# Kernel optimization log

Measured on AMD Instinct MI355X. Metric: run time of the kernel, lower is better.

## Reference

```python
import jax, jax.numpy as jnp
import numpy as np
import math

B, Hdim, Wdim = 8, 32, 32
CH = [64, 128, 256, 512]
KV = 960


def setup_inputs() -> dict:
    key = jax.random.key(0)
    ks = jax.random.split(key, 24)
    f32 = jnp.float32
    inp = {}
    inp["emb1"] = jax.random.normal(ks[0], (B, CH[0], Hdim, Wdim), f32)
    inp["emb2"] = jax.random.normal(ks[1], (B, CH[1], Hdim, Wdim), f32)
    inp["emb3"] = jax.random.normal(ks[2], (B, CH[2], Hdim, Wdim), f32)
    inp["emb4"] = jax.random.normal(ks[3], (B, CH[3], Hdim, Wdim), f32)
    inp["emb_all"] = jax.random.normal(ks[4], (B, KV, Hdim, Wdim), f32)
    s = 0.05  # small init so softmax/instnorm stay well-conditioned
    inp["w_mhead1"] = jax.random.normal(ks[5], (CH[0], CH[0]), f32) * s
    inp["w_mhead2"] = jax.random.normal(ks[6], (CH[1], CH[1]), f32) * s
    inp["w_mhead3"] = jax.random.normal(ks[7], (CH[2], CH[2]), f32) * s
    inp["w_mhead4"] = jax.random.normal(ks[8], (CH[3], CH[3]), f32) * s
    inp["w_mheadq"] = jax.random.normal(ks[9], (KV, KV), f32) * s
    inp["w_mheadk"] = jax.random.normal(ks[10], (KV, KV), f32) * s
    inp["w_mheadv"] = jax.random.normal(ks[11], (KV, KV), f32) * s
    inp["w_q1"] = jax.random.normal(ks[12], (CH[0], 2, 3, 3), f32) * s
    inp["w_q2"] = jax.random.normal(ks[13], (CH[1], 2, 3, 3), f32) * s
    inp["w_q3"] = jax.random.normal(ks[14], (CH[2], 2, 3, 3), f32) * s
    inp["w_q4"] = jax.random.normal(ks[15], (CH[3], 2, 3, 3), f32) * s
    inp["w_qc"] = jax.random.normal(ks[16], (KV, 1, 3, 3), f32) * s
    inp["w_kc"] = jax.random.normal(ks[17], (KV, 1, 3, 3), f32) * s
    inp["w_vc"] = jax.random.normal(ks[18], (KV, 1, 3, 3), f32) * s
    inp["w_proj1"] = jax.random.normal(ks[19], (CH[0], CH[0]), f32) * s
    inp["w_proj2"] = jax.random.normal(ks[20], (CH[1], CH[1]), f32) * s
    inp["w_proj3"] = jax.random.normal(ks[21], (CH[2], CH[2]), f32) * s
    inp["w_proj4"] = jax.random.normal(ks[22], (CH[3], CH[3]), f32) * s
    return inp


def conv1x1(x, w):
    # x: [b,c,h,w], w: [o,c] (1x1 conv, no bias)
    return jnp.einsum('bchw,oc->bohw', x, w)


def dwconv3x3(x, w, groups):
    # torch grouped conv: w [O, C//g, 3, 3]
    return jax.lax.conv_general_dilated(
        x, w, window_strides=(1, 1), padding='SAME',
        dimension_numbers=('NCHW', 'OIHW', 'NCHW'),
        feature_group_count=groups)


def l2norm(x):
    # F.normalize(dim=-1): divide by max(||x||_2, 1e-12)
    n = jnp.sqrt(jnp.sum(x * x, axis=-1, keepdims=True))
    return x / jnp.maximum(n, 1e-12)


def instnorm(x, eps=1e-5):
    # InstanceNorm2d(head=1, affine=False) on [b, head, c, n]: normalize per (b, head)
    m = jnp.mean(x, axis=(2, 3), keepdims=True)
    v = jnp.var(x, axis=(2, 3), keepdims=True)
    return (x - m) * jax.lax.rsqrt(v + eps)


def reference(emb1, emb2, emb3, emb4, emb_all,
              w_mhead1, w_mhead2, w_mhead3, w_mhead4,
              w_mheadq, w_mheadk, w_mheadv,
              w_q1, w_q2, w_q3, w_q4,
              w_qc, w_kc, w_vc,
              w_proj1, w_proj2, w_proj3, w_proj4):
    b, _, h, w = emb1.shape
    hw = h * w
    scale = 1.0 / math.sqrt(KV)

    # channel cross-attention over the concatenated features
    Qc = dwconv3x3(conv1x1(emb_all, w_mheadq), w_qc, KV).reshape(b, 1, KV, hw)
    Kc = dwconv3x3(conv1x1(emb_all, w_mheadk), w_kc, KV).reshape(b, 1, KV, hw)
    Vc = dwconv3x3(conv1x1(emb_all, w_mheadv), w_vc, KV).reshape(b, 1, KV, hw)
    Qc = l2norm(Qc)
    Kc = l2norm(Kc)
    sim = jnp.einsum('bhcn,bhdn->bhcd', Qc, Kc) * scale  # [b,1,KV,KV]
    sim = jax.nn.softmax(instnorm(sim), axis=-1)
    ctx = jnp.einsum('bhcd,bhdn->bhcn', sim, Vc)  # [b,1,KV,hw]

    def branch(emb, w_mh, w_q, groups, w_proj):
        c = emb.shape[1]
        q = dwconv3x3(conv1x1(emb, w_mh), w_q, groups).reshape(b, 1, c, hw)
        q = l2norm(q)
        attn = jnp.einsum('bhcn,bhdn->bhcd', q, ctx) * scale  # [b,1,c,KV]
        p = jax.nn.softmax(instnorm(attn), axis=-1)
        o = jnp.einsum('bhcd,bhdn->bhcn', p, ctx)  # [b,1,c,hw]
        o = jnp.mean(o, axis=1).reshape(b, c, h, w)
        return conv1x1(o, w_proj)

    O1 = branch(emb1, w_mhead1, w_q1, CH[0] // 2, w_proj1)
    O2 = branch(emb2, w_mhead2, w_q2, CH[1] // 2, w_proj2)
    O3 = branch(emb3, w_mhead3, w_q3, CH[2] // 2, w_proj3)
    O4 = branch(emb4, w_mhead4, w_q4, CH[3] // 2, w_proj4)
    return (O1, O2, O3, O4)
```

## Files before the change

### kernel.cpp

```cpp
#include <hip/hip_runtime.h>
#include <hip/hip_bf16.h>
#include <math.h>

#define NB 8
#define HWN 1024
#define KVC 960

typedef short bf16x8 __attribute__((ext_vector_type(8)));
typedef unsigned short u16x8 __attribute__((ext_vector_type(8)));
typedef float f32x4 __attribute__((ext_vector_type(4)));
typedef unsigned short ushort_t;

__device__ inline ushort_t f2bf(float f) {
    __hip_bfloat16 h = __float2bfloat16(f);
    return *reinterpret_cast<ushort_t*>(&h);
}
__device__ inline float bf2f(ushort_t u) {
    union { float f; unsigned int i; } x; x.i = ((unsigned int)u) << 16; return x.f;
}
__device__ inline int XB(int n) { return ((n & 7) ^ ((n >> 3) & 7)) << 1; }

__device__ inline void glds16(const ushort_t* src, ushort_t* dst) {
    __builtin_amdgcn_global_load_lds(
        (const __attribute__((address_space(1))) void*)src,
        (__attribute__((address_space(3))) void*)dst, 16, 0, 0);
}

struct F2BTab {
    const float* src[16];
    long dstOff[16];
    int nblk[16];
    int nseg;
};

__global__ __launch_bounds__(256)
void f2b_batched(F2BTab tab, ushort_t* base)
{
    int b = blockIdx.x, s = 0;
    while (s < tab.nseg - 1 && b >= tab.nblk[s]) { b -= tab.nblk[s]; ++s; }
    float4 v = *((const float4*)tab.src[s] + (long)b * 256 + threadIdx.x);
    ushort4 o = make_ushort4(f2bf(v.x), f2bf(v.y), f2bf(v.z), f2bf(v.w));
    *((ushort4*)(base + tab.dstOff[s]) + (long)b * 256 + threadIdx.x) = o;
}

__global__ __launch_bounds__(256)
void mfma_gemm_nt_stats(const ushort_t* __restrict__ A, const ushort_t* __restrict__ B,
                        float* __restrict__ C, float2* __restrict__ part,
                        int M, int N, int K, long sA, long sB, long sC, float alpha)
{
    __shared__ __align__(16) ushort_t lA[128 * 64];
    __shared__ __align__(16) ushort_t lB[128 * 64];
    const ushort_t* Ab = A + (long)blockIdx.z * sA;
    const ushort_t* Bb = B + (long)blockIdx.z * sB;
    const int row0 = blockIdx.y * 128, col0 = blockIdx.x * 128;
    const int t = threadIdx.x, lane = t & 63, w = t >> 6;
    const int wr = w >> 1, wc = w & 1;
    const int arl = lane >> 3;
    const int acs = ((lane & 7) ^ arl) * 8;
    int arow[4], brow[4];
    #pragma unroll
    for (int j = 0; j < 4; ++j) {
        int r = row0 + w * 32 + j * 8 + arl;  arow[j] = r < M ? r : M - 1;
        int rb = col0 + w * 32 + j * 8 + arl; brow[j] = rb < N ? rb : N - 1;
    }

    f32x4 acc[4][4];
    #pragma unroll
    for (int m = 0; m < 4; ++m)
        #pragma unroll
        for (int n = 0; n < 4; ++n)
            acc[m][n] = (f32x4){0.f, 0.f, 0.f, 0.f};

    for (int k0 = 0; k0 < K; k0 += 64) {
        #pragma unroll
        for (int j = 0; j < 4; ++j) {
            glds16(Ab + (long)arow[j] * K + k0 + acs, lA + (w * 32 + j * 8) * 64);
            glds16(Bb + (long)brow[j] * K + k0 + acs, lB + (w * 32 + j * 8) * 64);
        }
        __syncthreads();
        #pragma unroll
        for (int sub = 0; sub < 2; ++sub) {
            const int kc = (lane >> 4) + sub * 4;
            bf16x8 aF[4], bF[4];
            #pragma unroll
            for (int m = 0; m < 4; ++m) {
                int rl = wr * 64 + m * 16 + (lane & 15);
                aF[m] = *(const bf16x8*)(lA + rl * 64 + (kc ^ (rl & 7)) * 8);
            }
            #pragma unroll
            for (int n = 0; n < 4; ++n) {
                int rl = wc * 64 + n * 16 + (lane & 15);
                bF[n] = *(const bf16x8*)(lB + rl * 64 + (kc ^ (rl & 7)) * 8);
            }
            #pragma unroll
            for (int m = 0; m < 4; ++m)
                #pragma unroll
                for (int n = 0; n < 4; ++n)
                    acc[m][n] = __builtin_amdgcn_mfma_f32_16x16x32_bf16(aF[m], bF[n], acc[m][n], 0, 0, 0);
        }
        __syncthreads();
    }

    const int cr0 = row0 + wr * 64 + (lane >> 4) * 4;
    const int cc0 = col0 + wc * 64 + (lane & 15);
    float* Cb = C + (long)blockIdx.z * sC;
    float s1 = 0.f, s2 = 0.f;
    #pragma unroll
    for (int m = 0; m < 4; ++m) {
        #pragma unroll
        for (int n = 0; n < 4; ++n) {
            int ccol = cc0 + n * 16;
            if (ccol >= N) continue;
            #pragma unroll
            for (int r = 0; r < 4; ++r) {
                int crow = cr0 + m * 16 + r;
                if (crow < M) {
                    float v = acc[m][n][r] * alpha;
                    Cb[(long)crow * N + ccol] = v;
                    s1 += v; s2 += v * v;
                }
            }
        }
    }
    #pragma unroll
    for (int off = 32; off > 0; off >>= 1) {
        s1 += __shfl_down(s1, off);
        s2 += __shfl_down(s2, off);
    }
    float* rbuf = (float*)lA;
    if (lane == 0) { rbuf[w] = s1; rbuf[4 + w] = s2; }
    __syncthreads();
    if (t == 0)
        part[(blockIdx.z * 8 + blockIdx.y) * 8 + blockIdx.x] =
            make_float2(rbuf[0] + rbuf[1] + rbuf[2] + rbuf[3],
                        rbuf[4] + rbuf[5] + rbuf[6] + rbuf[7]);
}

struct NNTab {
    const ushort_t* A[5];
    const ushort_t* B[5];
    void* C[5];
    long sA[5], sB[5], sC[5];
    int M[5], K[5], obf[5], mt0[5];
    int nseg;
};

__global__ __launch_bounds__(256)
void mfma_gemm_nn(NNTab tab)
{
    __shared__ __align__(16) ushort_t lA[128 * 64];
    __shared__ __align__(16) ushort_t lB[128 * 64];
    int si = 0;
    #pragma unroll
    for (int s = 1; s < 5; ++s)
        if (s < tab.nseg && (int)blockIdx.y >= tab.mt0[s]) si = s;
    const int M = tab.M[si], K = tab.K[si];
    const int ytile = blockIdx.y - tab.mt0[si];
    const ushort_t* Ab = tab.A[si] + (long)blockIdx.z * tab.sA[si];
    const ushort_t* Bb = tab.B[si] + (long)blockIdx.z * tab.sB[si];
    const int row0 = ytile * 128, col0 = blockIdx.x * 128;
    const int t = threadIdx.x, lane = t & 63, w = t >> 6;
    const int wr = w >> 1, wc = w & 1;
    const int arl = lane >> 3;
    const int acs = ((lane & 7) ^ arl) * 8;
    int arow[4];
    #pragma unroll
    for (int j = 0; j < 4; ++j) {
        int r = row0 + w * 32 + j * 8 + arl;
        arow[j] = r < M ? r : M - 1;
    }
    const int n_i = t & 31, k_i = t >> 5;

    f32x4 acc[4][4];
    #pragma unroll
    for (int m = 0; m < 4; ++m)
        #pragma unroll
        for (int n = 0; n < 4; ++n)
            acc[m][n] = (f32x4){0.f, 0.f, 0.f, 0.f};

    for (int k0 = 0; k0 < K; k0 += 64) {
        #pragma unroll
        for (int j = 0; j < 4; ++j)
            glds16(Ab + (long)arow[j] * K + k0 + acs, lA + (w * 32 + j * 8) * 64);
        ushort4 q[8];
        const int gk = k0 + k_i * 8;
        #pragma unroll
        for (int kk = 0; kk < 8; ++kk)
            q[kk] = *(const ushort4*)(Bb + (long)(gk + kk) * 1024 + col0 + n_i * 4);
        #pragma unroll
        for (int i = 0; i < 4; ++i) {
            int n = n_i * 4 + i;
            int cw = (k_i * 2) ^ XB(n);
            u16x8 v;
            #pragma unroll
            for (int kk = 0; kk < 4; ++kk) {
                v[kk]     = ((const ushort_t*)&q[kk])[i];
                v[4 + kk] = ((const ushort_t*)&q[4 + kk])[i];
            }
            *(u16x8*)(lB + n * 64 + cw * 4) = v;
        }
        __syncthreads();
        #pragma unroll
        for (int sub = 0; sub < 2; ++sub) {
            const int kcA = (lane >> 4) + sub * 4;
            const int cB = (lane >> 4) * 2 + sub * 8;
            bf16x8 aF[4], bF[4];
            #pragma unroll
            for (int m = 0; m < 4; ++m) {
                int rl = wr * 64 + m * 16 + (lane & 15);
                aF[m] = *(const bf16x8*)(lA + rl * 64 + (kcA ^ (rl & 7)) * 8);
            }
            #pragma unroll
            for (int n = 0; n < 4; ++n) {
                int nl = wc * 64 + n * 16 + (lane & 15);
                bF[n] = *(const bf16x8*)(lB + nl * 64 + (cB ^ XB(nl)) * 4);
            }
            #pragma unroll
            for (int m = 0; m < 4; ++m)
                #pragma unroll
                for (int n = 0; n < 4; ++n)
                    acc[m][n] = __builtin_amdgcn_mfma_f32_16x16x32_bf16(aF[m], bF[n], acc[m][n], 0, 0, 0);
        }
        __syncthreads();
    }

    const int cr0 = row0 + wr * 64 + (lane >> 4) * 4;
    const int cc0 = col0 + wc * 64 + (lane & 15);
    const int obf = tab.obf[si];
    ushort_t* Cb_b = (ushort_t*)tab.C[si] + (long)blockIdx.z * tab.sC[si];
    float* Cb_f = (float*)tab.C[si] + (long)blockIdx.z * tab.sC[si];
    #pragma unroll
    for (int m = 0; m < 4; ++m) {
        #pragma unroll
        for (int n = 0; n < 4; ++n) {
            int ccol = cc0 + n * 16;
            #pragma unroll
            for (int r = 0; r < 4; ++r) {
                int crow = cr0 + m * 16 + r;
                if (crow < M) {
                    float v = acc[m][n][r];
                    if (obf) Cb_b[(long)crow * 1024 + ccol] = f2bf(v);
                    else     Cb_f[(long)crow * 1024 + ccol] = v;
                }
            }
        }
    }
}

__global__ __launch_bounds__(256)
void stencil_all(const ushort_t* __restrict__ Xqkv, const ushort_t* __restrict__ mh_x,
                 const float* __restrict__ w_qc, const float* __restrict__ w_kc,
                 const float* __restrict__ w_vc,
                 const float* __restrict__ wq1, const float* __restrict__ wq2,
                 const float* __restrict__ wq3, const float* __restrict__ wq4,
                 ushort_t* __restrict__ Qc, ushort_t* __restrict__ Kc,
                 ushort_t* __restrict__ Vc, ushort_t* __restrict__ q_all)
{
    __shared__ float p0[32 * 33];
    __shared__ float p1[32 * 33];
    __shared__ float red[5];
    const int bid = blockIdx.x;
    const int t = threadIdx.x;
    const int i0 = t * 4, y = i0 >> 5, x0 = i0 & 31;

    if (bid < 23040) {
        const int which = bid / 7680;
        const int p = bid - which * 7680;
        const int b = p / 960, c = p - b * 960;
        const ushort_t* ip = Xqkv + ((long)b * 2880 + which * 960 + c) * 1024;
        const float* wgt = (which == 0 ? w_qc : which == 1 ? w_kc : w_vc) + c * 9;
        ushort_t* op = (which == 0 ? Qc : which == 1 ? Kc : Vc) + (long)p * 1024;
        ushort4 u = *(const ushort4*)(ip + i0);
        float* rw = p0 + y * 33 + x0;
        rw[0] = bf2f(u.x); rw[1] = bf2f(u.y); rw[2] = bf2f(u.z); rw[3] = bf2f(u.w);
        __syncthreads();
        float W[9];
        #pragma unroll
        for (int q = 0; q < 9; ++q) W[q] = wgt[q];
        float r[3][6];
        #pragma unroll
        for (int dy = 0; dy < 3; ++dy) {
            int yy = y + dy - 1;
            bool vy = (unsigned)yy < 32u;
            #pragma unroll
            for (int j = 0; j < 6; ++j) {
                int xx = x0 - 1 + j;
                r[dy][j] = (vy && (unsigned)xx < 32u) ? p0[yy * 33 + xx] : 0.f;
            }
        }
        float o[4];
        #pragma unroll
        for (int q = 0; q < 4; ++q)
            o[q] = r[0][q] * W[0] + r[0][q + 1] * W[1] + r[0][q + 2] * W[2]
                 + r[1][q] * W[3] + r[1][q + 1] * W[4] + r[1][q + 2] * W[5]
                 + r[2][q] * W[6] + r[2][q + 1] * W[7] + r[2][q + 2] * W[8];
        float inv = 1.f;
        if (which < 2) {
            float s = o[0] * o[0] + o[1] * o[1] + o[2] * o[2] + o[3] * o[3];
            #pragma unroll
            for (int off = 32; off > 0; off >>= 1) s += __shfl_down(s, off);
            if ((t & 63) == 0) red[t >> 6] = s;
            __syncthreads();
            if (t == 0) red[4] = 1.0f / fmaxf(sqrtf(red[0] + red[1] + red[2] + red[3]), 1e-12f);
            __syncthreads();
            inv = red[4];
        }
        *(ushort4*)(op + i0) =
            make_ushort4(f2bf(o[0] * inv), f2bf(o[1] * inv), f2bf(o[2] * inv), f2bf(o[3] * inv));
        return;
    }
    const int po = bid - 23040;
    const int o = po & 1023, b = po >> 10;
    ushort_t* op = q_all + (long)po * 1024;
    int off; const float* wbase;
    if (o < 64)       { off = 0;   wbase = wq1; }
    else if (o < 128) { *(ushort4*)(op + i0) = make_ushort4(0, 0, 0, 0); return; }
    else if (o < 256) { off = 128; wbase = wq2; }
    else if (o < 512) { off = 256; wbase = wq3; }
    else              { off = 512; wbase = wq4; }
    const int ol = o - off;
    const int g2 = ol & ~1;
    const ushort_t* ip0 = mh_x + ((long)(b << 10) + off + g2) * 1024;
    const ushort_t* ip1 = ip0 + 1024;
    ushort4 u0 = *(const ushort4*)(ip0 + i0);
    ushort4 u1 = *(const ushort4*)(ip1 + i0);
    float* r0w = p0 + y * 33 + x0;
    float* r1w = p1 + y * 33 + x0;
    r0w[0] = bf2f(u0.x); r0w[1] = bf2f(u0.y); r0w[2] = bf2f(u0.z); r0w[3] = bf2f(u0.w);
    r1w[0] = bf2f(u1.x); r1w[1] = bf2f(u1.y); r1w[2] = bf2f(u1.z); r1w[3] = bf2f(u1.w);
    __syncthreads();
    const float* wp = wbase + ol * 18;
    float W[18];
    #pragma unroll
    for (int q = 0; q < 18; ++q) W[q] = wp[q];
    float o4[4] = {0.f, 0.f, 0.f, 0.f};
    #pragma unroll
    for (int pl = 0; pl < 2; ++pl) {
        const float* src = pl ? p1 : p0;
        const float* Wp = W + pl * 9;
        float r[3][6];
        #pragma unroll
        for (int dy = 0; dy < 3; ++dy) {
            int yy = y + dy - 1;
            bool vy = (unsigned)yy < 32u;
            #pragma unroll
            for (int j = 0; j < 6; ++j) {
                int xx = x0 - 1 + j;
                r[dy][j] = (vy && (unsigned)xx < 32u) ? src[yy * 33 + xx] : 0.f;
            }
        }
        #pragma unroll
        for (int q = 0; q < 4; ++q)
            o4[q] += r[0][q] * Wp[0] + r[0][q + 1] * Wp[1] + r[0][q + 2] * Wp[2]
                   + r[1][q] * Wp[3] + r[1][q + 1] * Wp[4] + r[1][q + 2] * Wp[5]
                   + r[2][q] * Wp[6] + r[2][q + 1] * Wp[7] + r[2][q + 2] * Wp[8];
    }
    float s = o4[0] * o4[0] + o4[1] * o4[1] + o4[2] * o4[2] + o4[3] * o4[3];
    #pragma unroll
    for (int off2 = 32; off2 > 0; off2 >>= 1) s += __shfl_down(s, off2);
    if ((t & 63) == 0) red[t >> 6] = s;
    __syncthreads();
    if (t == 0) red[4] = 1.0f / fmaxf(sqrtf(red[0] + red[1] + red[2] + red[3]), 1e-12f);
    __syncthreads();
    float inv = red[4];
    *(ushort4*)(op + i0) =
        make_ushort4(f2bf(o4[0] * inv), f2bf(o4[1] * inv), f2bf(o4[2] * inv), f2bf(o4[3] * inv));
}

__global__ void reduce_sim(const float2* __restrict__ part, float2* __restrict__ stats)
{
    float2 p = part[blockIdx.x * 64 + threadIdx.x];
    float s1 = p.x, s2 = p.y;
    #pragma unroll
    for (int off = 32; off > 0; off >>= 1) {
        s1 += __shfl_down(s1, off);
        s2 += __shfl_down(s2, off);
    }
    if (threadIdx.x == 0) stats[blockIdx.x] = make_float2(s1, s2);
}

__global__ void reduce_branch(const float2* __restrict__ part, float2* __restrict__ stats)
{
    const int br = blockIdx.x & 3, b = blockIdx.x >> 2;
    const int lo4[4] = {0, 1, 2, 4}, hi4[4] = {1, 2, 4, 8};
    float s1 = 0.f, s2 = 0.f;
    if (threadIdx.x < 8) {
        for (int my = lo4[br]; my < hi4[br]; ++my) {
            float2 p = part[(b * 8 + my) * 8 + threadIdx.x];
            s1 += p.x; s2 += p.y;
        }
    }
    #pragma unroll
    for (int off = 32; off > 0; off >>= 1) {
        s1 += __shfl_down(s1, off);
        s2 += __shfl_down(s2, off);
    }
    if (threadIdx.x == 0) stats[b * 4 + br] = make_float2(s1, s2);
}

__global__ __launch_bounds__(256)
void instnorm_softmax_bf16(const float* __restrict__ x, ushort_t* __restrict__ out,
                           const float2* __restrict__ stats, int rowsPerB, float invL)
{
    int row = blockIdx.x;
    int b = row / rowsPerB;
    float2 st = stats[b];
    float mean = st.x * invL;
    float var = st.y * invL - mean * mean;
    float rinv = rsqrtf(var + 1e-5f);
    const float* xr = x + (long)row * 960;
    ushort_t* orow = out + (long)row * 960;
    int t = threadIdx.x;
    float v[4];
    float mx = -1e30f;
    #pragma unroll
    for (int q = 0; q < 4; ++q) {
        int i = t + q * 256;
        if (i < 960) { v[q] = (xr[i] - mean) * rinv; mx = fmaxf(mx, v[q]); }
        else v[q] = -1e30f;
    }
    #pragma unroll
    for (int off = 32; off > 0; off >>= 1) mx = fmaxf(mx, __shfl_down(mx, off));
    __shared__ float rm[4];
    __shared__ float bmax, bsuminv;
    if ((t & 63) == 0) rm[t >> 6] = mx;
    __syncthreads();
    if (t == 0) bmax = fmaxf(fmaxf(rm[0], rm[1]), fmaxf(rm[2], rm[3]));
    __syncthreads();
    float mall = bmax;
    float s = 0.f;
    #pragma unroll
    for (int q = 0; q < 4; ++q) {
        int i = t + q * 256;
        if (i < 960) { v[q] = __expf(v[q] - mall); s += v[q]; }
    }
    #pragma unroll
    for (int off = 32; off > 0; off >>= 1) s += __shfl_down(s, off);
    if ((t & 63) == 0) rm[t >> 6] = s;
    __syncthreads();
    if (t == 0) bsuminv = 1.0f / (rm[0] + rm[1] + rm[2] + rm[3]);
    __syncthreads();
    float invS = bsuminv;
    #pragma unroll
    for (int q = 0; q < 4; ++q) {
        int i = t + q * 256;
        if (i < 960) orow[i] = f2bf(v[q] * invS);
    }
}

__global__ __launch_bounds__(256)
void softmax_attn_kernel(const float* __restrict__ x, ushort_t* __restrict__ P,
                         const float2* __restrict__ stats)
{
    const int r = blockIdx.x & 1023, b = blockIdx.x >> 10;
    const int t = threadIdx.x;
    ushort_t* orow = P + ((long)(b << 10) + r) * 960;
    int br; float cnt;
    if (r < 64)       { br = 0; cnt = 64.f; }
    else if (r < 128) {
        #pragma unroll
        for (int q = 0; q < 4; ++q) {
            int i = t + q * 256;
            if (i < 960) orow[i] = 0;
        }
        return;
    }
    else if (r < 256) { br = 1; cnt = 128.f; }
    else if (r < 512) { br = 2; cnt = 256.f; }
    else              { br = 3; cnt = 512.f; }
    float invL = 1.0f / (cnt * 960.f);
    float2 st = stats[b * 4 + br];
    float mean = st.x * invL;
    float var = st.y * invL - mean * mean;
    float rinv = rsqrtf(var + 1e-5f);
    const float* xr = x + ((long)(b << 10) + r) * 960;
    float v[4];
    float mx = -1e30f;
    #pragma unroll
    for (int q = 0; q < 4; ++q) {
        int i = t + q * 256;
        if (i < 960) { v[q] = (xr[i] - mean) * rinv; mx = fmaxf(mx, v[q]); }
        else v[q] = -1e30f;
    }
    #pragma unroll
    for (int off = 32; off > 0; off >>= 1) mx = fmaxf(mx, __shfl_down(mx, off));
    __shared__ float rm[4];
    __shared__ float bmax, bsuminv;
    if ((t & 63) == 0) rm[t >> 6] = mx;
    __syncthreads();
    if (t == 0) bmax = fmaxf(fmaxf(rm[0], rm[1]), fmaxf(rm[2], rm[3]));
    __syncthreads();
    float mall = bmax;
    float s = 0.f;
    #pragma unroll
    for (int q = 0; q < 4; ++q) {
        int i = t + q * 256;
        if (i < 960) { v[q] = __expf(v[q] - mall); s += v[q]; }
    }
    #pragma unroll
    for (int off = 32; off > 0; off >>= 1) s += __shfl_down(s, off);
    if ((t & 63) == 0) rm[t >> 6] = s;
    __syncthreads();
    if (t == 0) bsuminv = 1.0f / (rm[0] + rm[1] + rm[2] + rm[3]);
    __syncthreads();
    float invS = bsuminv;
    #pragma unroll
    for (int q = 0; q < 4; ++q) {
        int i = t + q * 256;
        if (i < 960) orow[i] = f2bf(v[q] * invS);
    }
}


extern "C" void kernel_launch(void* const* d_in, const int* in_sizes, int n_in,
                              void* d_out, int out_size, void* d_ws, size_t ws_size,
                              hipStream_t stream)
{
    const float* emb[4]  = {(const float*)d_in[0], (const float*)d_in[1],
                            (const float*)d_in[2], (const float*)d_in[3]};
    const float* emb_all = (const float*)d_in[4];
    const float* w_mh[4] = {(const float*)d_in[5], (const float*)d_in[6],
                            (const float*)d_in[7], (const float*)d_in[8]};
    const float* w_mq = (const float*)d_in[9];
    const float* w_mk = (const float*)d_in[10];
    const float* w_mv = (const float*)d_in[11];
    const float* w_q[4] = {(const float*)d_in[12], (const float*)d_in[13],
                           (const float*)d_in[14], (const float*)d_in[15]};
    const float* w_qc = (const float*)d_in[16];
    const float* w_kc = (const float*)d_in[17];
    const float* w_vc = (const float*)d_in[18];
    const float* w_proj[4] = {(const float*)d_in[19], (const float*)d_in[20],
                              (const float*)d_in[21], (const float*)d_in[22]};
    float* out = (float*)d_out;

    char* Wb = (char*)d_ws;
    ushort_t* U = (ushort_t*)d_ws;
    const long eWQKV = 0;
    const long eWMH  = 2764800;
    const long eWPJ  = 3112960;
    const long eEmbA = 3461120;
    const long eEmbI = 11325440;
    const long eXq   = 19189760;
    const long eMhx  = 42782720;
    const long eQc   = 51171328;
    const long eKc   = 59035648;
    const long eVc   = 66899968;
    const long eF6   = eXq;
    const long ePc   = eXq + 15728640;
    const long eQall = eEmbA;
    const long eCtx  = eMhx;
    const long ePall = eQc;
    const long eOall = eKc;
    float2* part  = (float2*)(Wb + 149528576);
    float2* stats = (float2*)(Wb + 149533000);

    ushort_t* WQKVb = U + eWQKV;
    ushort_t* WMHb  = U + eWMH;
    ushort_t* WPJb  = U + eWPJ;
    ushort_t* embB_all = U + eEmbA;
    ushort_t* Xqkv  = U + eXq;
    ushort_t* mh_x  = U + eMhx;
    ushort_t* QcB   = U + eQc;
    ushort_t* KcB   = U + eKc;
    ushort_t* VcB   = U + eVc;
    float*    F6    = (float*)(U + eF6);
    ushort_t* Pc    = U + ePc;
    ushort_t* q_all = U + eQall;
    ushort_t* ctx   = U + eCtx;
    ushort_t* P_all = U + ePall;
    ushort_t* o_all = U + eOall;
    ushort_t* embB_i[4] = {U + eEmbI, U + eEmbI + 524288, U + eEmbI + 1572864, U + eEmbI + 3670016};

    const float scale = 0.0322748612183951400f;
    const long SB = (long)KVC * HWN;
    const long S1024 = 1024L * 1024;
    const int CH[4] = {64, 128, 256, 512};
    const int mhoff[4] = {0, 4096, 20480, 86016};
    const int rowOff[4] = {0, 128, 256, 512};
    const long outOff[4] = {0, 524288, 1572864, 3670016};
    dim3 blk(256);

    F2BTab tf;
    const float* fs[16] = {w_mq, w_mk, w_mv,
                           w_mh[0], w_mh[1], w_mh[2], w_mh[3],
                           w_proj[0], w_proj[1], w_proj[2], w_proj[3],
                           emb_all, emb[0], emb[1], emb[2], emb[3]};
    long fd[16] = {eWQKV, eWQKV + 921600, eWQKV + 1843200,
                   eWMH + 0, eWMH + 4096, eWMH + 20480, eWMH + 86016,
                   eWPJ + 0, eWPJ + 4096, eWPJ + 20480, eWPJ + 86016,
                   eEmbA, eEmbI, eEmbI + 524288, eEmbI + 1572864, eEmbI + 3670016};
    int fn[16] = {900, 900, 900, 4, 16, 64, 256, 4, 16, 64, 256,
                  7680, 512, 1024, 2048, 4096};
    int ftot = 0;
    for (int i = 0; i < 16; ++i) { tf.src[i] = fs[i]; tf.dstOff[i] = fd[i]; tf.nblk[i] = fn[i]; ftot += fn[i]; }
    tf.nseg = 16;
    f2b_batched<<<ftot, blk, 0, stream>>>(tf, U);

    auto nn1 = [&](const ushort_t* A, long sA, const ushort_t* B, long sB,
                   void* C, long sC, int M, int K, int obf) {
        NNTab tb;
        tb.A[0] = A; tb.B[0] = B; tb.C[0] = C;
        tb.sA[0] = sA; tb.sB[0] = sB; tb.sC[0] = sC;
        tb.M[0] = M; tb.K[0] = K; tb.obf[0] = obf; tb.mt0[0] = 0;
        for (int s = 1; s < 5; ++s) { tb.A[s] = A; tb.B[s] = B; tb.C[s] = C; tb.sA[s] = 0; tb.sB[s] = 0; tb.sC[s] = 0; tb.M[s] = M; tb.K[s] = K; tb.obf[s] = obf; tb.mt0[s] = 1 << 30; }
        tb.nseg = 1;
        dim3 g(8, (M + 127) / 128, NB);
        mfma_gemm_nn<<<g, blk, 0, stream>>>(tb);
    };

    {
        NNTab tb;
        tb.A[0] = WQKVb; tb.B[0] = embB_all; tb.C[0] = Xqkv;
        tb.sA[0] = 0; tb.sB[0] = SB; tb.sC[0] = 2880L * 1024;
        tb.M[0] = 2880; tb.K[0] = 960; tb.obf[0] = 1; tb.mt0[0] = 0;
        int mt = 23;
        for (int i = 0; i < 4; ++i) {
            tb.A[1 + i] = WMHb + mhoff[i]; tb.B[1 + i] = embB_i[i];
            tb.C[1 + i] = mh_x + (long)rowOff[i] * 1024;
            tb.sA[1 + i] = 0; tb.sB[1 + i] = (long)CH[i] * 1024; tb.sC[1 + i] = S1024;
            tb.M[1 + i] = CH[i]; tb.K[1 + i] = CH[i]; tb.obf[1 + i] = 1; tb.mt0[1 + i] = mt;
            mt += (CH[i] + 127) / 128;
        }
        tb.nseg = 5;
        dim3 g(8, mt, NB);
        mfma_gemm_nn<<<g, blk, 0, stream>>>(tb);
    }

    stencil_all<<<31232, blk, 0, stream>>>(Xqkv, mh_x, w_qc, w_kc, w_vc,
                                           w_q[0], w_q[1], w_q[2], w_q[3],
                                           QcB, KcB, VcB, q_all);

    mfma_gemm_nt_stats<<<dim3(8, 8, NB), blk, 0, stream>>>(
        QcB, KcB, F6, part, KVC, KVC, HWN, SB, SB, (long)KVC * KVC, scale);
    reduce_sim<<<NB, 64, 0, stream>>>(part, stats);
    instnorm_softmax_bf16<<<NB * KVC, blk, 0, stream>>>(F6, Pc, stats, KVC,
                                                        1.f / ((float)KVC * (float)KVC));

    nn1(Pc, (long)KVC * KVC, VcB, SB, ctx, SB, KVC, KVC, 1);

    mfma_gemm_nt_stats<<<dim3(8, 8, NB), blk, 0, stream>>>(
        q_all, ctx, F6, part, 1024, KVC, HWN, S1024, SB, SB, scale);
    reduce_branch<<<32, 64, 0, stream>>>(part, stats);
    softmax_attn_kernel<<<NB * 1024, blk, 0, stream>>>(F6, P_all, stats);

    nn1(P_all, SB, ctx, SB, o_all, S1024, 1024, KVC, 1);

    {
        NNTab tb;
        int mt = 0;
        for (int i = 0; i < 4; ++i) {
            tb.A[i] = WPJb + mhoff[i]; tb.B[i] = o_all + (long)rowOff[i] * 1024;
            tb.C[i] = out + outOff[i];
            tb.sA[i] = 0; tb.sB[i] = S1024; tb.sC[i] = (long)CH[i] * 1024;
            tb.M[i] = CH[i]; tb.K[i] = CH[i]; tb.obf[i] = 0; tb.mt0[i] = mt;
            mt += (CH[i] + 127) / 128;
        }
        tb.A[4] = tb.A[3]; tb.B[4] = tb.B[3]; tb.C[4] = tb.C[3];
        tb.sA[4] = 0; tb.sB[4] = 0; tb.sC[4] = 0;
        tb.M[4] = 1; tb.K[4] = 64; tb.obf[4] = 0; tb.mt0[4] = 1 << 30;
        tb.nseg = 4;
        dim3 g(8, mt, NB);
        mfma_gemm_nn<<<g, blk, 0, stream>>>(tb);
    }

    (void)in_sizes; (void)n_in; (void)out_size; (void)ws_size;
}
```

Baseline: 331.2 us.

## Convert NN GEMMs to NT form with pre-transposed B operands

Replaces the NN GEMM, which transposed B in registers before writing to LDS, with an NT GEMM that loads both operands directly into LDS via global_load_lds. To make this possible, the embeddings are transposed during fp32-to-bf16 conversion, and Vc and ctx are transposed by new tiled transpose kernels. The final attention GEMM is reformulated to produce o transposed, so the projection can consume it as K-contiguous. Workspace buffers are re-aliased to fit the new intermediates. The cost is two extra transpose kernel launches and additional memory traffic.

```diff
diff --git a/kernel.cpp b/kernel.cpp
--- a/kernel.cpp
+++ b/kernel.cpp
@@ -7,7 +7,6 @@
 #define KVC 960
 
 typedef short bf16x8 __attribute__((ext_vector_type(8)));
-typedef unsigned short u16x8 __attribute__((ext_vector_type(8)));
 typedef float f32x4 __attribute__((ext_vector_type(4)));
 typedef unsigned short ushort_t;
 
@@ -18,8 +17,6 @@
 __device__ inline float bf2f(ushort_t u) {
     union { float f; unsigned int i; } x; x.i = ((unsigned int)u) << 16; return x.f;
 }
-__device__ inline int XB(int n) { return ((n & 7) ^ ((n >> 3) & 7)) << 1; }
-
 __device__ inline void glds16(const ushort_t* src, ushort_t* dst) {
     __builtin_amdgcn_global_load_lds(
         (const __attribute__((address_space(1))) void*)src,
@@ -27,9 +24,9 @@
 }
 
 struct F2BTab {
-    const float* src[16];
-    long dstOff[16];
-    int nblk[16];
+    const float* src[12];
+    long dstOff[12];
+    int nblk[12];
     int nseg;
 };
 
@@ -41,6 +38,78 @@
     float4 v = *((const float4*)tab.src[s] + (long)b * 256 + threadIdx.x);
     ushort4 o = make_ushort4(f2bf(v.x), f2bf(v.y), f2bf(v.z), f2bf(v.w));
     *((ushort4*)(base + tab.dstOff[s]) + (long)b * 256 + threadIdx.x) = o;
+}
+
+struct F2TTab {
+    const float* src[5];
+    long dstOff[5];
+    long sIn[5], sOut[5];
+    int R[5];
+    int nblk[5];
+    int nseg;
+};
+
+__global__ __launch_bounds__(256)
+void f2bt_batched(F2TTab tab, ushort_t* base)
+{
+    __shared__ ushort_t tile[64][65];
+    int b = blockIdx.x, s = 0;
+    while (s < tab.nseg - 1 && b >= tab.nblk[s]) { b -= tab.nblk[s]; ++s; }
+    const int R = tab.R[s];
+    const int tpb = (R >> 6) * 16;
+    const int batch = b / tpb, rem = b - batch * tpb;
+    const int rtile = rem >> 4, ctile = rem & 15;
+    const float* ib = tab.src[s] + (long)batch * tab.sIn[s] + (long)(rtile * 64) * 1024 + ctile * 64;
+    const int t = threadIdx.x, tr = t >> 4, tc = (t & 15) * 4;
+    #pragma unroll
+    for (int p = 0; p < 4; ++p) {
+        float4 v = *(const float4*)(ib + (long)(tr + 16 * p) * 1024 + tc);
+        tile[tr + 16 * p][tc + 0] = f2bf(v.x);
+        tile[tr + 16 * p][tc + 1] = f2bf(v.y);
+        tile[tr + 16 * p][tc + 2] = f2bf(v.z);
+        tile[tr + 16 * p][tc + 3] = f2bf(v.w);
+    }
+    __syncthreads();
+    ushort_t* ob = base + tab.dstOff[s] + (long)batch * tab.sOut[s]
+                 + (long)(ctile * 64) * R + rtile * 64;
+    #pragma unroll
+    for (int p = 0; p < 4; ++p) {
+        ushort4 v;
+        v.x = tile[tc + 0][tr + 16 * p];
+        v.y = tile[tc + 1][tr + 16 * p];
+        v.z = tile[tc + 2][tr + 16 * p];
+        v.w = tile[tc + 3][tr + 16 * p];
+        *(ushort4*)(ob + (long)(tr + 16 * p) * R + tc) = v;
+    }
+}
+
+__global__ __launch_bounds__(256)
+void trb_kernel(const ushort_t* __restrict__ in, ushort_t* __restrict__ out)
+{
+    __shared__ ushort_t tile[64][65];
+    const int r0 = blockIdx.y * 64, c0 = blockIdx.x * 64;
+    const long sP = (long)KVC * HWN;
+    const ushort_t* ib = in + (long)blockIdx.z * sP;
+    ushort_t* ob = out + (long)blockIdx.z * sP;
+    const int t = threadIdx.x, tr = t >> 4, tc = (t & 15) * 4;
+    #pragma unroll
+    for (int p = 0; p < 4; ++p) {
+        ushort4 v = *(const ushort4*)(ib + (long)(r0 + tr + 16 * p) * 1024 + c0 + tc);
+        tile[tr + 16 * p][tc + 0] = v.x;
+        tile[tr + 16 * p][tc + 1] = v.y;
+        tile[tr + 16 * p][tc + 2] = v.z;
+        tile[tr + 16 * p][tc + 3] = v.w;
+    }
+    __syncthreads();
+    #pragma unroll
+    for (int p = 0; p < 4; ++p) {
+        ushort4 v;
+        v.x = tile[tc + 0][tr + 16 * p];
+        v.y = tile[tc + 1][tr + 16 * p];
+        v.z = tile[tc + 2][tr + 16 * p];
+        v.w = tile[tc + 3][tr + 16 * p];
+        *(ushort4*)(ob + (long)(c0 + tr + 16 * p) * 960 + r0 + tc) = v;
+    }
 }
 
 __global__ __launch_bounds__(256)
@@ -136,17 +205,17 @@
                         rbuf[4] + rbuf[5] + rbuf[6] + rbuf[7]);
 }
 
-struct NNTab {
+struct NTTab {
     const ushort_t* A[5];
     const ushort_t* B[5];
     void* C[5];
-    long sA[5], sB[5], sC[5];
+    long sA[5], sB[5], sC[5], ldb[5];
     int M[5], K[5], obf[5], mt0[5];
     int nseg;
 };
 
 __global__ __launch_bounds__(256)
-void mfma_gemm_nn(NNTab tab)
+void mfma_gemm_nt_tab(NTTab tab)
 {
     __shared__ __align__(16) ushort_t lA[128 * 64];
     __shared__ __align__(16) ushort_t lB[128 * 64];
@@ -155,21 +224,21 @@
     for (int s = 1; s < 5; ++s)
         if (s < tab.nseg && (int)blockIdx.y >= tab.mt0[s]) si = s;
     const int M = tab.M[si], K = tab.K[si];
-    const int ytile = blockIdx.y - tab.mt0[si];
+    const long ldb = tab.ldb[si];
     const ushort_t* Ab = tab.A[si] + (long)blockIdx.z * tab.sA[si];
     const ushort_t* Bb = tab.B[si] + (long)blockIdx.z * tab.sB[si];
-    const int row0 = ytile * 128, col0 = blockIdx.x * 128;
+    const int row0 = (blockIdx.y - tab.mt0[si]) * 128, col0 = blockIdx.x * 128;
     const int t = threadIdx.x, lane = t & 63, w = t >> 6;
     const int wr = w >> 1, wc = w & 1;
     const int arl = lane >> 3;
     const int acs = ((lane & 7) ^ arl) * 8;
-    int arow[4];
+    int arow[4], brow[4];
     #pragma unroll
     for (int j = 0; j < 4; ++j) {
         int r = row0 + w * 32 + j * 8 + arl;
         arow[j] = r < M ? r : M - 1;
-    }
-    const int n_i = t & 31, k_i = t >> 5;
+        brow[j] = col0 + w * 32 + j * 8 + arl;
+    }
 
     f32x4 acc[4][4];
     #pragma unroll
@@ -180,40 +249,24 @@
 
     for (int k0 = 0; k0 < K; k0 += 64) {
         #pragma unroll
-        for (int j = 0; j < 4; ++j)
+        for (int j = 0; j < 4; ++j) {
             glds16(Ab + (long)arow[j] * K + k0 + acs, lA + (w * 32 + j * 8) * 64);
-        ushort4 q[8];
-        const int gk = k0 + k_i * 8;
-        #pragma unroll
-        for (int kk = 0; kk < 8; ++kk)
-            q[kk] = *(const ushort4*)(Bb + (long)(gk + kk) * 1024 + col0 + n_i * 4);
-        #pragma unroll
-        for (int i = 0; i < 4; ++i) {
-            int n = n_i * 4 + i;
-            int cw = (k_i * 2) ^ XB(n);
-            u16x8 v;
-            #pragma unroll
-            for (int kk = 0; kk < 4; ++kk) {
-                v[kk]     = ((const ushort_t*)&q[kk])[i];
-                v[4 + kk] = ((const ushort_t*)&q[4 + kk])[i];
-            }
-            *(u16x8*)(lB + n * 64 + cw * 4) = v;
+            glds16(Bb + (long)brow[j] * ldb + k0 + acs, lB + (w * 32 + j * 8) * 64);
         }
         __syncthreads();
         #pragma unroll
         for (int sub = 0; sub < 2; ++sub) {
-            const int kcA = (lane >> 4) + sub * 4;
-            const int cB = (lane >> 4) * 2 + sub * 8;
+            const int kc = (lane >> 4) + sub * 4;
             bf16x8 aF[4], bF[4];
             #pragma unroll
             for (int m = 0; m < 4; ++m) {
                 int rl = wr * 64 + m * 16 + (lane & 15);
-                aF[m] = *(const bf16x8*)(lA + rl * 64 + (kcA ^ (rl & 7)) * 8);
+                aF[m] = *(const bf16x8*)(lA + rl * 64 + (kc ^ (rl & 7)) * 8);
             }
             #pragma unroll
             for (int n = 0; n < 4; ++n) {
-                int nl = wc * 64 + n * 16 + (lane & 15);
-                bF[n] = *(const bf16x8*)(lB + nl * 64 + (cB ^ XB(nl)) * 4);
+                int rl = wc * 64 + n * 16 + (lane & 15);
+                bF[n] = *(const bf16x8*)(lB + rl * 64 + (kc ^ (rl & 7)) * 8);
             }
             #pragma unroll
             for (int m = 0; m < 4; ++m)
@@ -533,43 +586,39 @@
                               (const float*)d_in[21], (const float*)d_in[22]};
     float* out = (float*)d_out;
 
-    char* Wb = (char*)d_ws;
     ushort_t* U = (ushort_t*)d_ws;
     const long eWQKV = 0;
     const long eWMH  = 2764800;
     const long eWPJ  = 3112960;
-    const long eEmbA = 3461120;
-    const long eEmbI = 11325440;
-    const long eXq   = 19189760;
-    const long eMhx  = 42782720;
+    const long eR1   = 3461120;
+    const long eR2   = 11325440;
+    const long eR3   = 19189760;
+    const long ePc   = 34918400;
+    const long eR4   = 42782720;
     const long eQc   = 51171328;
     const long eKc   = 59035648;
-    const long eVc   = 66899968;
-    const long eF6   = eXq;
-    const long ePc   = eXq + 15728640;
-    const long eQall = eEmbA;
-    const long eCtx  = eMhx;
-    const long ePall = eQc;
-    const long eOall = eKc;
-    float2* part  = (float2*)(Wb + 149528576);
-    float2* stats = (float2*)(Wb + 149533000);
+    const long eQall = 66899968;
+    float2* part  = (float2*)(U + 75288576);
+    float2* stats = part + 512;
 
     ushort_t* WQKVb = U + eWQKV;
     ushort_t* WMHb  = U + eWMH;
     ushort_t* WPJb  = U + eWPJ;
-    ushort_t* embB_all = U + eEmbA;
-    ushort_t* Xqkv  = U + eXq;
-    ushort_t* mh_x  = U + eMhx;
+    ushort_t* embT_all = U + eR1;
+    ushort_t* Vc    = U + eR1;
+    ushort_t* ctx   = U + eR1;
+    ushort_t* VcT   = U + eR2;
+    ushort_t* ctxT  = U + eR2;
+    ushort_t* Xqkv  = U + eR3;
+    float*    S6    = (float*)(U + eR3);
+    ushort_t* oT    = U + eR3;
+    ushort_t* Pc    = U + ePc;
+    ushort_t* mh_x  = U + eR4;
+    ushort_t* P_all = U + eR4;
     ushort_t* QcB   = U + eQc;
     ushort_t* KcB   = U + eKc;
-    ushort_t* VcB   = U + eVc;
-    float*    F6    = (float*)(U + eF6);
-    ushort_t* Pc    = U + ePc;
     ushort_t* q_all = U + eQall;
-    ushort_t* ctx   = U + eCtx;
-    ushort_t* P_all = U + ePall;
-    ushort_t* o_all = U + eOall;
-    ushort_t* embB_i[4] = {U + eEmbI, U + eEmbI + 524288, U + eEmbI + 1572864, U + eEmbI + 3670016};
+    ushort_t* embT_i[4] = {U + eR2, U + eR2 + 524288, U + eR2 + 1572864, U + eR2 + 3670016};
 
     const float scale = 0.0322748612183951400f;
     const long SB = (long)KVC * HWN;
@@ -580,87 +629,109 @@
     const long outOff[4] = {0, 524288, 1572864, 3670016};
     dim3 blk(256);
 
-    F2BTab tf;
-    const float* fs[16] = {w_mq, w_mk, w_mv,
-                           w_mh[0], w_mh[1], w_mh[2], w_mh[3],
-                           w_proj[0], w_proj[1], w_proj[2], w_proj[3],
-                           emb_all, emb[0], emb[1], emb[2], emb[3]};
-    long fd[16] = {eWQKV, eWQKV + 921600, eWQKV + 1843200,
-                   eWMH + 0, eWMH + 4096, eWMH + 20480, eWMH + 86016,
-                   eWPJ + 0, eWPJ + 4096, eWPJ + 20480, eWPJ + 86016,
-                   eEmbA, eEmbI, eEmbI + 524288, eEmbI + 1572864, eEmbI + 3670016};
-    int fn[16] = {900, 900, 900, 4, 16, 64, 256, 4, 16, 64, 256,
-                  7680, 512, 1024, 2048, 4096};
-    int ftot = 0;
-    for (int i = 0; i < 16; ++i) { tf.src[i] = fs[i]; tf.dstOff[i] = fd[i]; tf.nblk[i] = fn[i]; ftot += fn[i]; }
-    tf.nseg = 16;
-    f2b_batched<<<ftot, blk, 0, stream>>>(tf, U);
-
-    auto nn1 = [&](const ushort_t* A, long sA, const ushort_t* B, long sB,
+    {
+        F2BTab tf;
+        const float* fs[11] = {w_mq, w_mk, w_mv, w_mh[0], w_mh[1], w_mh[2], w_mh[3],
+                               w_proj[0], w_proj[1], w_proj[2], w_proj[3]};
+        long fd[11] = {eWQKV, eWQKV + 921600, eWQKV + 1843200,
+                       eWMH + 0, eWMH + 4096, eWMH + 20480, eWMH + 86016,
+                       eWPJ + 0, eWPJ + 4096, eWPJ + 20480, eWPJ + 86016};
+        int fn[11] = {900, 900, 900, 4, 16, 64, 256, 4, 16, 64, 256};
+        int ftot = 0;
+        for (int i = 0; i < 11; ++i) { tf.src[i] = fs[i]; tf.dstOff[i] = fd[i]; tf.nblk[i] = fn[i]; ftot += fn[i]; }
+        tf.nseg = 11;
+        f2b_batched<<<ftot, blk, 0, stream>>>(tf, U);
+    }
+    {
+        F2TTab tt;
+        const float* ts[5] = {emb_all, emb[0], emb[1], emb[2], emb[3]};
+        long td[5] = {eR1, eR2, eR2 + 524288, eR2 + 1572864, eR2 + 3670016};
+        int tR[5] = {960, 64, 128, 256, 512};
+        int tn[5];
+        long tsi[5], tso[5];
+        int ttot = 0;
+        for (int i = 0; i < 5; ++i) {
+            tsi[i] = (long)tR[i] * 1024; tso[i] = tsi[i];
+            tn[i] = NB * (tR[i] / 64) * 16; ttot += tn[i];
+            tt.src[i] = ts[i]; tt.dstOff[i] = td[i]; tt.R[i] = tR[i];
+            tt.sIn[i] = tsi[i]; tt.sOut[i] = tso[i]; tt.nblk[i] = tn[i];
+        }
+        tt.nseg = 5;
+        f2bt_batched<<<ttot, blk, 0, stream>>>(tt, U);
+    }
+
+    auto nt1 = [&](const ushort_t* A, long sA, const ushort_t* B, long sB, long ldb,
                    void* C, long sC, int M, int K, int obf) {
-        NNTab tb;
-        tb.A[0] = A; tb.B[0] = B; tb.C[0] = C;
-        tb.sA[0] = sA; tb.sB[0] = sB; tb.sC[0] = sC;
-        tb.M[0] = M; tb.K[0] = K; tb.obf[0] = obf; tb.mt0[0] = 0;
-        for (int s = 1; s < 5; ++s) { tb.A[s] = A; tb.B[s] = B; tb.C[s] = C; tb.sA[s] = 0; tb.sB[s] = 0; tb.sC[s] = 0; tb.M[s] = M; tb.K[s] = K; tb.obf[s] = obf; tb.mt0[s] = 1 << 30; }
+        NTTab tb;
+        for (int s = 0; s < 5; ++s) {
+            tb.A[s] = A; tb.B[s] = B; tb.C[s] = C;
+            tb.sA[s] = sA; tb.sB[s] = sB; tb.sC[s] = sC; tb.ldb[s] = ldb;
+            tb.M[s] = M; tb.K[s] = K; tb.obf[s] = obf; tb.mt0[s] = (s == 0) ? 0 : (1 << 30);
+        }
         tb.nseg = 1;
         dim3 g(8, (M + 127) / 128, NB);
-        mfma_gemm_nn<<<g, blk, 0, stream>>>(tb);
+        mfma_gemm_nt_tab<<<g, blk, 0, stream>>>(tb);
     };
 
     {
-        NNTab tb;
-        tb.A[0] = WQKVb; tb.B[0] = embB_all; tb.C[0] = Xqkv;
-        tb.sA[0] = 0; tb.sB[0] = SB; tb.sC[0] = 2880L * 1024;
+        NTTab tb;
+        tb.A[0] = WQKVb; tb.B[0] = embT_all; tb.C[0] = Xqkv;
+        tb.sA[0] = 0; tb.sB[0] = SB; tb.sC[0] = 2880L * 1024; tb.ldb[0] = 960;
         tb.M[0] = 2880; tb.K[0] = 960; tb.obf[0] = 1; tb.mt0[0] = 0;
         int mt = 23;
         for (int i = 0; i < 4; ++i) {
-            tb.A[1 + i] = WMHb + mhoff[i]; tb.B[1 + i] = embB_i[i];
+            tb.A[1 + i] = WMHb + mhoff[i]; tb.B[1 + i] = embT_i[i];
             tb.C[1 + i] = mh_x + (long)rowOff[i] * 1024;
             tb.sA[1 + i] = 0; tb.sB[1 + i] = (long)CH[i] * 1024; tb.sC[1 + i] = S1024;
+            tb.ldb[1 + i] = CH[i];
             tb.M[1 + i] = CH[i]; tb.K[1 + i] = CH[i]; tb.obf[1 + i] = 1; tb.mt0[1 + i] = mt;
             mt += (CH[i] + 127) / 128;
         }
         tb.nseg = 5;
         dim3 g(8, mt, NB);
-        mfma_gemm_nn<<<g, blk, 0, stream>>>(tb);
+        mfma_gemm_nt_tab<<<g, blk, 0, stream>>>(tb);
     }
 
     stencil_all<<<31232, blk, 0, stream>>>(Xqkv, mh_x, w_qc, w_kc, w_vc,
                                            w_q[0], w_q[1], w_q[2], w_q[3],
-                                           QcB, KcB, VcB, q_all);
+                                           QcB, KcB, Vc, q_all);
+
+    trb_kernel<<<dim3(16, 15, NB), blk, 0, stream>>>(Vc, VcT);
 
     mfma_gemm_nt_stats<<<dim3(8, 8, NB), blk, 0, stream>>>(
-        QcB, KcB, F6, part, KVC, KVC, HWN, SB, SB, (long)KVC * KVC, scale);
+        QcB, KcB, S6, part, KVC, KVC, HWN, SB, SB, (long)KVC * KVC, scale);
     reduce_sim<<<NB, 64, 0, stream>>>(part, stats);
-    instnorm_softmax_bf16<<<NB * KVC, blk, 0, stream>>>(F6, Pc, stats, KVC,
+    instnorm_softmax_bf16<<<NB * KVC, blk, 0, stream>>>(S6, Pc, stats, KVC,
                                                         1.f / ((float)KVC * (float)KVC));
 
-    nn1(Pc, (long)KVC * KVC, VcB, SB, ctx, SB, KVC, KVC, 1);
+    nt1(Pc, (long)KVC * KVC, VcT, SB, 960, ctx, SB, KVC, KVC, 1);
+
+    trb_kernel<<<dim3(16, 15, NB), blk, 0, stream>>>(ctx, ctxT);
 
     mfma_gemm_nt_stats<<<dim3(8, 8, NB), blk, 0, stream>>>(
-        q_all, ctx, F6, part, 1024, KVC, HWN, S1024, SB, SB, scale);
+        q_all, ctx, S6, part, 1024, KVC, HWN, S1024, SB, SB, scale);
     reduce_branch<<<32, 64, 0, stream>>>(part, stats);
-    softmax_attn_kernel<<<NB * 1024, blk, 0, stream>>>(F6, P_all, stats);
-
-    nn1(P_all, SB, ctx, SB, o_all, S1024, 1024, KVC, 1);
+    softmax_attn_kernel<<<NB * 1024, blk, 0, stream>>>(S6, P_all, stats);
+
+    nt1(ctxT, SB, P_all, SB, 960, oT, S1024, 1024, KVC, 1);
 
     {
-        NNTab tb;
+        NTTab tb;
         int mt = 0;
         for (int i = 0; i < 4; ++i) {
-            tb.A[i] = WPJb + mhoff[i]; tb.B[i] = o_all + (long)rowOff[i] * 1024;
+            tb.A[i] = WPJb + mhoff[i]; tb.B[i] = oT + rowOff[i];
             tb.C[i] = out + outOff[i];
             tb.sA[i] = 0; tb.sB[i] = S1024; tb.sC[i] = (long)CH[i] * 1024;
+            tb.ldb[i] = 1024;
             tb.M[i] = CH[i]; tb.K[i] = CH[i]; tb.obf[i] = 0; tb.mt0[i] = mt;
             mt += (CH[i] + 127) / 128;
         }
         tb.A[4] = tb.A[3]; tb.B[4] = tb.B[3]; tb.C[4] = tb.C[3];
-        tb.sA[4] = 0; tb.sB[4] = 0; tb.sC[4] = 0;
+        tb.sA[4] = 0; tb.sB[4] = 0; tb.sC[4] = 0; tb.ldb[4] = 1024;
         tb.M[4] = 1; tb.K[4] = 64; tb.obf[4] = 0; tb.mt0[4] = 1 << 30;
         tb.nseg = 4;
         dim3 g(8, mt, NB);
-        mfma_gemm_nn<<<g, blk, 0, stream>>>(tb);
+        mfma_gemm_nt_tab<<<g, blk, 0, stream>>>(tb);
     }
 
     (void)in_sizes; (void)n_in; (void)out_size; (void)ws_size;
```

Result: no change. 330.9 us (-0.1%).
